# Kernel tuning notes

Measured on AMD Instinct MI355X. Metric: run time of the kernel, lower is better.

Reference implementation:

```python
import jax, jax.numpy as jnp
import numpy as np

DIM = 256
D_STATE = 32
EXPAND = 2
E = EXPAND * DIM            # d_inner = 512
DT_RANK = (DIM + 15) // 16  # 16 (mamba default ceil(d_model/16))
D_CONV = 4                  # mamba default causal conv width
B = 4
L = 1024


def layernorm(x, g, b, eps=1e-5):
    m = jnp.mean(x, axis=-1, keepdims=True)
    v = jnp.var(x, axis=-1, keepdims=True)
    return (x - m) / jnp.sqrt(v + eps) * g + b


def dwconv(x_bcl, w, b, pad):
    # x_bcl: [B,C,L], w: [C,1,K] depthwise
    y = jax.lax.conv_general_dilated(
        x_bcl, w, window_strides=(1,), padding=[pad],
        feature_group_count=x_bcl.shape[1],
        dimension_numbers=('NCW', 'OIW', 'NCW'))
    return y + b[None, :, None]


def selective_scan(u, dt, A, Bm, Cm, D):
    # u,dt: [B,L,E]; A: [E,N]; Bm,Cm: [B,L,N]; D: [E]
    dA = jnp.exp(dt[..., None] * A)                                # [B,L,E,N]
    dBu = dt[..., None] * Bm[:, :, None, :] * u[..., None]         # [B,L,E,N]

    def step(h, inp):
        dA_t, dBu_t = inp
        h = dA_t * h + dBu_t
        return h, h

    h0 = jnp.zeros((u.shape[0], E, D_STATE), u.dtype)
    _, hs = jax.lax.scan(step, h0, (dA.transpose(1, 0, 2, 3), dBu.transpose(1, 0, 2, 3)))
    y = jnp.einsum('lben,bln->ble', hs, Cm)                        # [B,L,E]
    return y + u * D


def mamba(x, in_proj_w, ssm_conv_w, ssm_conv_b, x_proj_w,
          dt_proj_w, dt_proj_b, A_log, Dp, out_proj_w):
    xz = x @ in_proj_w.T                     # [B,L,2E]
    xin, z = xz[..., :E], xz[..., E:]
    # causal depthwise conv (pad left D_CONV-1) + SiLU
    xc = dwconv(xin.transpose(0, 2, 1), ssm_conv_w, ssm_conv_b, (D_CONV - 1, 0))
    u = jax.nn.silu(xc).transpose(0, 2, 1)   # [B,L,E]
    dbl = u @ x_proj_w.T                      # [B,L,dt_rank+2N]
    dt_r = dbl[..., :DT_RANK]
    Bm = dbl[..., DT_RANK:DT_RANK + D_STATE]
    Cm = dbl[..., DT_RANK + D_STATE:]
    dt = jax.nn.softplus(dt_r @ dt_proj_w.T + dt_proj_b)  # [B,L,E]
    A = -jnp.exp(A_log)                                    # [E,N]
    y = selective_scan(u, dt, A, Bm, Cm, Dp)
    y = y * jax.nn.silu(z)
    return y @ out_proj_w.T


def setup_inputs() -> dict:
    key = jax.random.key(0)
    ks = jax.random.split(key, 12)
    f = lambda k, s, sc=0.02: jax.random.normal(k, s, jnp.float32) * sc
    dt_init = jnp.exp(jax.random.uniform(ks[10], (E,), jnp.float32,
                                         np.log(1e-3), np.log(1e-1)))
    dt_bias = dt_init + jnp.log(-jnp.expm1(-dt_init))  # inverse softplus
    A_log = jnp.log(jnp.tile(jnp.arange(1, D_STATE + 1, dtype=jnp.float32), (E, 1)))
    return {
        'x': jax.random.normal(ks[0], (B, L, DIM), jnp.float32),
        'norm1_g': jnp.ones((DIM,), jnp.float32), 'norm1_b': jnp.zeros((DIM,), jnp.float32),
        'conv_w': f(ks[1], (DIM, 1, 3), 0.1), 'conv_b': jnp.zeros((DIM,), jnp.float32),
        'in_proj_w': f(ks[2], (2 * E, DIM)),
        'ssm_conv_w': f(ks[3], (E, 1, D_CONV), 0.1), 'ssm_conv_b': jnp.zeros((E,), jnp.float32),
        'x_proj_w': f(ks[4], (DT_RANK + 2 * D_STATE, E)),
        'dt_proj_w': f(ks[5], (E, DT_RANK), 0.1), 'dt_proj_b': dt_bias,
        'A_log': A_log, 'Dp': jnp.ones((E,), jnp.float32),
        'out_proj_w': f(ks[6], (DIM, E)),
        'norm2_g': jnp.ones((DIM,), jnp.float32), 'norm2_b': jnp.zeros((DIM,), jnp.float32),
        'mlp_w1': f(ks[7], (4 * DIM, DIM)), 'mlp_b1': jnp.zeros((4 * DIM,), jnp.float32),
        'mlp_w2': f(ks[8], (DIM, 4 * DIM)), 'mlp_b2': jnp.zeros((DIM,), jnp.float32),
    }


def reference(x, norm1_g, norm1_b, conv_w, conv_b, in_proj_w, ssm_conv_w,
              ssm_conv_b, x_proj_w, dt_proj_w, dt_proj_b, A_log, Dp,
              out_proj_w, norm2_g, norm2_b, mlp_w1, mlp_b1, mlp_w2, mlp_b2):
    res = x
    h = layernorm(x, norm1_g, norm1_b)
    # local depthwise conv, kernel 3, same padding
    h_conv = dwconv(h.transpose(0, 2, 1), conv_w, conv_b, (1, 1)).transpose(0, 2, 1)
    h = mamba(h_conv + h, in_proj_w, ssm_conv_w, ssm_conv_b, x_proj_w,
              dt_proj_w, dt_proj_b, A_log, Dp, out_proj_w)
    h = res + h  # drop_path = identity (eval)
    m = layernorm(h, norm2_g, norm2_b)
    m = jax.nn.gelu(m @ mlp_w1.T + mlp_b1, approximate=False) @ mlp_w2.T + mlp_b2
    return h + m
```

## Files before the change

### kernel.cpp

```cpp
#include <hip/hip_runtime.h>
#include <hip/hip_bf16.h>
#include <math.h>

#define BATCH 4
#define LSEQ  1024
#define DIM   256
#define ESZ   512
#define NST   32
#define RNK   16
#define MROWS 4096
#define NCH   64
#define CHL   16

typedef __attribute__((ext_vector_type(8))) short bf16x8;
typedef __attribute__((ext_vector_type(4))) float f32x4;

__device__ __forceinline__ float silu_f(float v) { return v / (1.f + __expf(-v)); }
__device__ __forceinline__ float softplus_f(float v) {
    return (v > 20.f) ? v : log1pf(__expf(v));
}

__global__ __launch_bounds__(256) void prep_kernel(
    const float* __restrict__ ipw, const float* __restrict__ opw,
    const float* __restrict__ w1,  const float* __restrict__ w2,
    const float* __restrict__ xpw, __hip_bfloat16* __restrict__ dst,
    const float* __restrict__ x, const float* __restrict__ g,
    const float* __restrict__ b, const float* __restrict__ cw,
    const float* __restrict__ cb, __hip_bfloat16* __restrict__ hm)
{
    if (blockIdx.x < 936) {
        int i = blockIdx.x * 256 + threadIdx.x;
        if (i >= 239616) return;
        const float* s; int off;
        if      (i < 65536)  { s = ipw; off = i; }
        else if (i < 98304)  { s = opw; off = i - 65536; }
        else if (i < 163840) { s = w1;  off = i - 98304; }
        else if (i < 229376) { s = w2;  off = i - 163840; }
        else                 { s = xpw; off = i - 229376; }
        float4 v = ((const float4*)s)[off];
        union { __hip_bfloat16 h[4]; short4 s4; } u;
        u.h[0] = __float2bfloat16(v.x);
        u.h[1] = __float2bfloat16(v.y);
        u.h[2] = __float2bfloat16(v.z);
        u.h[3] = __float2bfloat16(v.w);
        ((short4*)dst)[i] = u.s4;
        return;
    }
    const int row = blockIdx.x - 936;
    const int l   = row & (LSEQ - 1);
    const int d   = threadIdx.x;
    const float gc = g[d], bc = b[d];

    float xc = x[row * DIM + d];
    float xl = (l > 0)        ? x[(row - 1) * DIM + d] : 0.f;
    float xr = (l < LSEQ - 1) ? x[(row + 1) * DIM + d] : 0.f;

    float a[6] = { xc, xc * xc, xl, xl * xl, xr, xr * xr };
    #pragma unroll
    for (int o = 32; o > 0; o >>= 1)
        #pragma unroll
        for (int j = 0; j < 6; ++j) a[j] += __shfl_down(a[j], o, 64);
    __shared__ float red[4][6];
    if ((d & 63) == 0)
        #pragma unroll
        for (int j = 0; j < 6; ++j) red[d >> 6][j] = a[j];
    __syncthreads();
    float t[6];
    #pragma unroll
    for (int j = 0; j < 6; ++j)
        t[j] = red[0][j] + red[1][j] + red[2][j] + red[3][j];

    auto ln = [&](float v, float s, float s2) {
        float m  = s * (1.f / DIM);
        float vr = s2 * (1.f / DIM) - m * m;
        return (v - m) * rsqrtf(vr + 1e-5f) * gc + bc;
    };
    float ln_c = ln(xc, t[0], t[1]);
    float acc  = cw[d * 3 + 1] * ln_c + cb[d] + ln_c;
    if (l > 0)        acc += cw[d * 3 + 0] * ln(xl, t[2], t[3]);
    if (l < LSEQ - 1) acc += cw[d * 3 + 2] * ln(xr, t[4], t[5]);
    hm[row * DIM + d] = __float2bfloat16(acc);
}

__global__ __launch_bounds__(256) void ln_kernel(
    const float* __restrict__ x, const float* __restrict__ g,
    const float* __restrict__ b, __hip_bfloat16* __restrict__ y)
{
    const int row = blockIdx.x;
    const int tid = threadIdx.x;
    float v = x[row * DIM + tid];
    float s = v, s2 = v * v;
    #pragma unroll
    for (int o = 32; o > 0; o >>= 1) {
        s  += __shfl_down(s,  o, 64);
        s2 += __shfl_down(s2, o, 64);
    }
    __shared__ float ls[4], ls2[4];
    if ((tid & 63) == 0) { ls[tid >> 6] = s; ls2[tid >> 6] = s2; }
    __syncthreads();
    float ts  = ls[0]  + ls[1]  + ls[2]  + ls[3];
    float ts2 = ls2[0] + ls2[1] + ls2[2] + ls2[3];
    float mean = ts * (1.f / DIM);
    float var  = ts2 * (1.f / DIM) - mean * mean;
    float inv  = rsqrtf(var + 1e-5f);
    y[row * DIM + tid] =
        __float2bfloat16((v - mean) * inv * g[tid] + b[tid]);
}

__global__ __launch_bounds__(256) void conv4_silu_kernel(
    const __hip_bfloat16* __restrict__ xz, const float* __restrict__ w,
    const float* __restrict__ cb, __hip_bfloat16* __restrict__ ub)
{
    const int i  = blockIdx.x * 256 + threadIdx.x;
    const int e  = i & (ESZ - 1);
    const int bl = i >> 9;
    const int l  = bl & (LSEQ - 1);
    float acc = cb[e];
    #pragma unroll
    for (int k = 0; k < 4; ++k) {
        int ls = l + k - 3;
        if (ls >= 0)
            acc += w[e * 4 + k] * __bfloat162float(xz[(long)(bl + k - 3) * 1024 + e]);
    }
    ub[(long)bl * ESZ + e] = __float2bfloat16(silu_f(acc));
}

__global__ __launch_bounds__(256) void dt_kernel(
    const float* __restrict__ dbl, const float* __restrict__ dtw,
    const float* __restrict__ dtb, __hip_bfloat16* __restrict__ dtf)
{
    const int row = blockIdx.x;
    __shared__ float dr[RNK];
    if (threadIdx.x < RNK) dr[threadIdx.x] = dbl[(long)row * 80 + threadIdx.x];
    __syncthreads();
    #pragma unroll
    for (int hh = 0; hh < 2; ++hh) {
        const int e = threadIdx.x + hh * 256;
        float raw = dtb[e];
        #pragma unroll
        for (int qd = 0; qd < 4; ++qd) {
            float4 w4 = *(const float4*)(dtw + e * RNK + qd * 4);
            raw += w4.x * dr[qd * 4 + 0] + w4.y * dr[qd * 4 + 1]
                 + w4.z * dr[qd * 4 + 2] + w4.w * dr[qd * 4 + 3];
        }
        dtf[(long)row * ESZ + e] = __float2bfloat16(softplus_f(raw));
    }
}

#define EPI_NONE      0
#define EPI_GELU      2
#define EPI_RES       3
#define EPI_BIAS_RES  4

template <int BM, int BN, int EPI, int OUT_BF16>
__global__ __launch_bounds__(256) void gemm_lds(
    const __hip_bfloat16* __restrict__ A, int lda,
    const __hip_bfloat16* __restrict__ W, int ldw,
    void* __restrict__ Cout, int ldc, int K,
    const float* __restrict__ bias,
    const float* __restrict__ res, int ldres)
{
    constexpr int BK  = 64;
    constexpr int WTN = BN / 4;
    constexpr int BNF = WTN / 16;
    constexpr int AMF = BM / 16;
    constexpr int AIT = (BM * 8) / 256;
    constexpr int WIT = (BN * 8) / 256;

    __shared__ __hip_bfloat16 As[2][BM * BK];
    __shared__ __hip_bfloat16 Ws[2][BN * BK];

    const int tid  = threadIdx.x;
    const int lane = tid & 63;
    const int wave = tid >> 6;
    const int wn   = wave * WTN;
    const int m0   = blockIdx.x * BM;
    const int n0   = blockIdx.y * BN;
    const int q    = lane >> 4;
    const int lr   = lane & 15;

    const __hip_bfloat16* Ab = A + (long)m0 * lda;
    const __hip_bfloat16* Wb = W + (long)n0 * ldw;

    f32x4 acc[AMF][BNF];
    #pragma unroll
    for (int i = 0; i < AMF; ++i)
        #pragma unroll
        for (int j = 0; j < BNF; ++j)
            acc[i][j] = (f32x4){0.f, 0.f, 0.f, 0.f};

    auto stage = [&](int s, int k0) {
        #pragma unroll
        for (int it = 0; it < AIT; ++it) {
            const int g = it * 256 + tid;
            __builtin_amdgcn_global_load_lds(
                (const __attribute__((address_space(1))) void*)
                    (Ab + (long)(g >> 3) * lda + k0 + (g & 7) * 8),
                (__attribute__((address_space(3))) void*)
                    (&As[s][(it * 256 + wave * 64) * 8]),
                16, 0, 0);
        }
        #pragma unroll
        for (int it = 0; it < WIT; ++it) {
            const int g = it * 256 + tid;
            __builtin_amdgcn_global_load_lds(
                (const __attribute__((address_space(1))) void*)
                    (Wb + (long)(g >> 3) * ldw + k0 + (g & 7) * 8),
                (__attribute__((address_space(3))) void*)
                    (&Ws[s][(it * 256 + wave * 64) * 8]),
                16, 0, 0);
        }
    };

    stage(0, 0);
    __syncthreads();

    int cur = 0;
    for (int k0 = 0; k0 < K; k0 += BK) {
        if (k0 + BK < K) stage(cur ^ 1, k0 + BK);
        #pragma unroll
        for (int ks = 0; ks < 2; ++ks) {
            bf16x8 af[AMF], bfr[BNF];
            #pragma unroll
            for (int i = 0; i < AMF; ++i)
                af[i] = *(const bf16x8*)(&As[cur][(i * 16 + lr) * BK + ks * 32 + q * 8]);
            #pragma unroll
            for (int j = 0; j < BNF; ++j)
                bfr[j] = *(const bf16x8*)(&Ws[cur][(wn + j * 16 + lr) * BK + ks * 32 + q * 8]);
            #pragma unroll
            for (int i = 0; i < AMF; ++i)
                #pragma unroll
                for (int j = 0; j < BNF; ++j)
                    acc[i][j] = __builtin_amdgcn_mfma_f32_16x16x32_bf16(
                        af[i], bfr[j], acc[i][j], 0, 0, 0);
        }
        __syncthreads();
        cur ^= 1;
    }

    #pragma unroll
    for (int i = 0; i < AMF; ++i) {
        #pragma unroll
        for (int j = 0; j < BNF; ++j) {
            const int col  = n0 + wn + j * 16 + lr;
            const int rowb = m0 + i * 16 + q * 4;
            #pragma unroll
            for (int r = 0; r < 4; ++r) {
                const int row = rowb + r;
                float v = acc[i][j][r];
                if (EPI == EPI_GELU) {
                    v += bias[col];
                    v = 0.5f * v * (1.f + erff(v * 0.70710678118654752f));
                } else if (EPI == EPI_RES) {
                    v += res[(long)row * ldres + col];
                } else if (EPI == EPI_BIAS_RES) {
                    v += bias[col] + res[(long)row * ldres + col];
                }
                if (OUT_BF16)
                    ((__hip_bfloat16*)Cout)[(long)row * ldc + col] = __float2bfloat16(v);
                else
                    ((float*)Cout)[(long)row * ldc + col] = v;
            }
        }
    }
}

__global__ __launch_bounds__(256) void xproj_mfma(
    const __hip_bfloat16* __restrict__ A,
    const __hip_bfloat16* __restrict__ W,
    float* __restrict__ C)
{
    constexpr int LS = 72;
    __shared__ __hip_bfloat16 As[64 * LS];
    __shared__ __hip_bfloat16 Ws[80 * LS];
    const int tid  = threadIdx.x;
    const int lane = tid & 63;
    const int wave = tid >> 6;
    const int wm   = wave * 16;
    const int m0   = blockIdx.x * 64;
    const int srow = tid >> 3;
    const int scol = (tid & 7) * 8;
    const int q    = lane >> 4;
    const int lr   = lane & 15;

    f32x4 acc[5];
    #pragma unroll
    for (int j = 0; j < 5; ++j) acc[j] = (f32x4){0.f, 0.f, 0.f, 0.f};

    float4 ar[2], wr[3];
    #pragma unroll
    for (int r = 0; r < 2; ++r)
        ar[r] = *(const float4*)(A + (long)(m0 + r * 32 + srow) * 512 + scol);
    #pragma unroll
    for (int r = 0; r < 3; ++r) {
        int row = r * 32 + srow;
        wr[r] = (row < 80) ? *(const float4*)(W + (long)row * 512 + scol)
                           : make_float4(0.f, 0.f, 0.f, 0.f);
    }

    for (int k0 = 0; k0 < 512; k0 += 64) {
        __syncthreads();
        #pragma unroll
        for (int r = 0; r < 2; ++r)
            *(float4*)(&As[(r * 32 + srow) * LS + scol]) = ar[r];
        #pragma unroll
        for (int r = 0; r < 3; ++r) {
            int row = r * 32 + srow;
            if (row < 80) *(float4*)(&Ws[row * LS + scol]) = wr[r];
        }
        __syncthreads();
        if (k0 + 64 < 512) {
            #pragma unroll
            for (int r = 0; r < 2; ++r)
                ar[r] = *(const float4*)(A + (long)(m0 + r * 32 + srow) * 512 + k0 + 64 + scol);
            #pragma unroll
            for (int r = 0; r < 3; ++r) {
                int row = r * 32 + srow;
                if (row < 80)
                    wr[r] = *(const float4*)(W + (long)row * 512 + k0 + 64 + scol);
            }
        }
        #pragma unroll
        for (int ks = 0; ks < 2; ++ks) {
            bf16x8 af = *(const bf16x8*)(&As[(wm + lr) * LS + ks * 32 + q * 8]);
            #pragma unroll
            for (int j = 0; j < 5; ++j) {
                bf16x8 bf = *(const bf16x8*)(&Ws[(j * 16 + lr) * LS + ks * 32 + q * 8]);
                acc[j] = __builtin_amdgcn_mfma_f32_16x16x32_bf16(af, bf, acc[j], 0, 0, 0);
            }
        }
    }
    #pragma unroll
    for (int j = 0; j < 5; ++j)
        #pragma unroll
        for (int r = 0; r < 4; ++r)
            C[(long)(m0 + wm + q * 4 + r) * 80 + j * 16 + lr] = acc[j][r];
}

__global__ __launch_bounds__(256) void scan_s1(
    const __hip_bfloat16* __restrict__ xz, const float* __restrict__ dbl,
    const __hip_bfloat16* __restrict__ dtf, const float* __restrict__ A_log,
    const float* __restrict__ scw, const float* __restrict__ scb,
    __hip_bfloat16* __restrict__ P, __hip_bfloat16* __restrict__ Q)
{
    const int tid = threadIdx.x;
    const int e  = ((blockIdx.x & 1) << 8) + tid;
    const int bc = blockIdx.x >> 1;
    const int c  = bc & (NCH - 1);
    const int b  = bc >> 6;

    __shared__ float sBC[CHL][64];
    {
        const int r  = tid >> 4;
        const int cg = (tid & 15) * 4;
        *(float4*)&sBC[r][cg] =
            *(const float4*)(dbl + ((long)b * LSEQ + c * CHL + r) * 80 + 16 + cg);
    }

    float Aen[NST];
    #pragma unroll
    for (int qd = 0; qd < 8; ++qd) {
        float4 a4 = *(const float4*)(A_log + e * NST + qd * 4);
        Aen[qd * 4 + 0] = -__expf(a4.x);
        Aen[qd * 4 + 1] = -__expf(a4.y);
        Aen[qd * 4 + 2] = -__expf(a4.z);
        Aen[qd * 4 + 3] = -__expf(a4.w);
    }
    float cw4[4];
    #pragma unroll
    for (int k = 0; k < 4; ++k) cw4[k] = scw[e * 4 + k];
    const float cbe = scb[e];

    const int l0 = c * CHL;
    const long rowbase = ((long)b * LSEQ) * 1024 + e;
    float xw0, xw1, xw2;
    if (c == 0) { xw0 = xw1 = xw2 = 0.f; }
    else {
        xw0 = __bfloat162float(xz[rowbase + (long)(l0 - 3) * 1024]);
        xw1 = __bfloat162float(xz[rowbase + (long)(l0 - 2) * 1024]);
        xw2 = __bfloat162float(xz[rowbase + (long)(l0 - 1) * 1024]);
    }

    float Pv[NST], Qv[NST];
    #pragma unroll
    for (int n = 0; n < NST; ++n) { Pv[n] = 1.f; Qv[n] = 0.f; }
    __syncthreads();

    for (int t = 0; t < CHL; ++t) {
        const int l = l0 + t;
        const long bl = (long)b * LSEQ + l;
        float xw3 = __bfloat162float(xz[rowbase + (long)l * 1024]);
        float u = silu_f(cbe + cw4[0]*xw0 + cw4[1]*xw1 + cw4[2]*xw2 + cw4[3]*xw3);
        xw0 = xw1; xw1 = xw2; xw2 = xw3;

        float dt = __bfloat162float(dtf[bl * ESZ + e]);
        float xx = dt * u;

        #pragma unroll
        for (int qd = 0; qd < 8; ++qd) {
            float4 b4 = *(const float4*)&sBC[t][qd * 4];
            #pragma unroll
            for (int j = 0; j < 4; ++j) {
                const int n = qd * 4 + j;
                float bn = (j == 0) ? b4.x : (j == 1) ? b4.y : (j == 2) ? b4.z : b4.w;
                float dA = __expf(dt * Aen[n]);
                Pv[n] *= dA;
                Qv[n] = fmaf(dA, Qv[n], xx * bn);
            }
        }
    }
    const long pb = ((long)(b * NCH + c) * NST) * ESZ + e;
    #pragma unroll
    for (int n = 0; n < NST; ++n) {
        P[pb + (long)n * ESZ] = __float2bfloat16(Pv[n]);
        Q[pb + (long)n * ESZ] = __float2bfloat16(Qv[n]);
    }
}

__global__ __launch_bounds__(256) void scan_s2(
    __hip_bfloat16* __restrict__ P, const __hip_bfloat16* __restrict__ Q)
{
    const int tg = blockIdx.x * 256 + threadIdx.x;
    const int e  = tg & (ESZ - 1);
    const int n  = (tg >> 9) & (NST - 1);
    const int b  = tg >> 14;
    float h = 0.f;
    #pragma unroll 4
    for (int c = 0; c < NCH; ++c) {
        const long idx = ((long)(b * NCH + c) * NST + n) * ESZ + e;
        float Pv = __bfloat162float(P[idx]);
        float Qv = __bfloat162float(Q[idx]);
        P[idx] = __float2bfloat16(h);
        h = fmaf(Pv, h, Qv);
    }
}

__global__ __launch_bounds__(256) void scan_s3(
    const __hip_bfloat16* __restrict__ xz, const float* __restrict__ dbl,
    const __hip_bfloat16* __restrict__ dtf, const float* __restrict__ A_log,
    const float* __restrict__ scw, const float* __restrict__ scb,
    const float* __restrict__ Dp, const __hip_bfloat16* __restrict__ H,
    __hip_bfloat16* __restrict__ yg)
{
    const int tid = threadIdx.x;
    const int e  = ((blockIdx.x & 1) << 8) + tid;
    const int bc = blockIdx.x >> 1;
    const int c  = bc & (NCH - 1);
    const int b  = bc >> 6;

    __shared__ float sBC[CHL][64];
    {
        const int r  = tid >> 4;
        const int cg = (tid & 15) * 4;
        *(float4*)&sBC[r][cg] =
            *(const float4*)(dbl + ((long)b * LSEQ + c * CHL + r) * 80 + 16 + cg);
    }

    float Aen[NST];
    #pragma unroll
    for (int qd = 0; qd < 8; ++qd) {
        float4 a4 = *(const float4*)(A_log + e * NST + qd * 4);
        Aen[qd * 4 + 0] = -__expf(a4.x);
        Aen[qd * 4 + 1] = -__expf(a4.y);
        Aen[qd * 4 + 2] = -__expf(a4.z);
        Aen[qd * 4 + 3] = -__expf(a4.w);
    }
    float cw4[4];
    #pragma unroll
    for (int k = 0; k < 4; ++k) cw4[k] = scw[e * 4 + k];
    const float cbe = scb[e];
    const float dpe = Dp[e];

    float h[NST];
    const long pb = ((long)(b * NCH + c) * NST) * ESZ + e;
    #pragma unroll
    for (int n = 0; n < NST; ++n)
        h[n] = __bfloat162float(H[pb + (long)n * ESZ]);

    const int l0 = c * CHL;
    const long rowbase = ((long)b * LSEQ) * 1024 + e;
    float xw0, xw1, xw2;
    if (c == 0) { xw0 = xw1 = xw2 = 0.f; }
    else {
        xw0 = __bfloat162float(xz[rowbase + (long)(l0 - 3) * 1024]);
        xw1 = __bfloat162float(xz[rowbase + (long)(l0 - 2) * 1024]);
        xw2 = __bfloat162float(xz[rowbase + (long)(l0 - 1) * 1024]);
    }
    __syncthreads();

    for (int t = 0; t < CHL; ++t) {
        const int l = l0 + t;
        const long bl = (long)b * LSEQ + l;
        float xw3 = __bfloat162float(xz[rowbase + (long)l * 1024]);
        float u = silu_f(cbe + cw4[0]*xw0 + cw4[1]*xw1 + cw4[2]*xw2 + cw4[3]*xw3);
        xw0 = xw1; xw1 = xw2; xw2 = xw3;

        float dt = __bfloat162float(dtf[bl * ESZ + e]);
        float xx = dt * u;

        float y = 0.f;
        #pragma unroll
        for (int qd = 0; qd < 8; ++qd) {
            float4 b4 = *(const float4*)&sBC[t][qd * 4];
            float4 c4 = *(const float4*)&sBC[t][32 + qd * 4];
            #pragma unroll
            for (int j = 0; j < 4; ++j) {
                const int n = qd * 4 + j;
                float bn = (j == 0) ? b4.x : (j == 1) ? b4.y : (j == 2) ? b4.z : b4.w;
                float cn = (j == 0) ? c4.x : (j == 1) ? c4.y : (j == 2) ? c4.z : c4.w;
                float dA = __expf(dt * Aen[n]);
                h[n] = fmaf(dA, h[n], xx * bn);
                y = fmaf(h[n], cn, y);
            }
        }
        y += u * dpe;
        float z = __bfloat162float(xz[rowbase + (long)l * 1024 + ESZ]);
        yg[bl * ESZ + e] = __float2bfloat16(y * silu_f(z));
    }
}

extern "C" void kernel_launch(void* const* d_in, const int* in_sizes, int n_in,
                              void* d_out, int out_size, void* d_ws, size_t ws_size,
                              hipStream_t stream)
{
    const float* x    = (const float*)d_in[0];
    const float* n1g  = (const float*)d_in[1];
    const float* n1b  = (const float*)d_in[2];
    const float* cw   = (const float*)d_in[3];
    const float* cb   = (const float*)d_in[4];
    const float* ipw  = (const float*)d_in[5];
    const float* scw  = (const float*)d_in[6];
    const float* scb  = (const float*)d_in[7];
    const float* xpw  = (const float*)d_in[8];
    const float* dtw  = (const float*)d_in[9];
    const float* dtbi = (const float*)d_in[10];
    const float* alog = (const float*)d_in[11];
    const float* dp   = (const float*)d_in[12];
    const float* opw  = (const float*)d_in[13];
    const float* n2g  = (const float*)d_in[14];
    const float* n2b  = (const float*)d_in[15];
    const float* w1   = (const float*)d_in[16];
    const float* b1   = (const float*)d_in[17];
    const float* w2   = (const float*)d_in[18];
    const float* b2   = (const float*)d_in[19];
    float* out = (float*)d_out;

    float* ws = (float*)d_ws;
    __hip_bfloat16* hmb  = (__hip_bfloat16*)(ws + 0);
    __hip_bfloat16* xzb  = (__hip_bfloat16*)(ws + 524288);
    __hip_bfloat16* ub   = (__hip_bfloat16*)(ws + 2621440);
    float*          dbl  = ws + 3670016;
    __hip_bfloat16* dtf  = (__hip_bfloat16*)(ws + 3997696);
    __hip_bfloat16* P    = (__hip_bfloat16*)(ws + 5046272);
    __hip_bfloat16* Q    = (__hip_bfloat16*)(ws + 7143424);
    __hip_bfloat16* ygb  = (__hip_bfloat16*)(ws + 9240576);
    float*          hres = ws + 10289152;
    __hip_bfloat16* h1b  = (__hip_bfloat16*)(ws + 11337728);
    __hip_bfloat16* midb = (__hip_bfloat16*)(ws + 11862016);
    __hip_bfloat16* wb   = (__hip_bfloat16*)(ws + 13959168);
    __hip_bfloat16* ipwb = wb;
    __hip_bfloat16* opwb = wb + 262144;
    __hip_bfloat16* w1b  = wb + 393216;
    __hip_bfloat16* w2b  = wb + 655360;
    __hip_bfloat16* xpwb = wb + 917504;

    prep_kernel<<<5032, 256, 0, stream>>>(ipw, opw, w1, w2, xpw, wb,
                                          x, n1g, n1b, cw, cb, hmb);
    gemm_lds<64, 128, EPI_NONE, 1><<<dim3(64, 8), 256, 0, stream>>>(
        hmb, 256, ipwb, 256, xzb, 1024, 256, nullptr, nullptr, 0);
    conv4_silu_kernel<<<8192, 256, 0, stream>>>(xzb, scw, scb, ub);
    xproj_mfma<<<64, 256, 0, stream>>>(ub, xpwb, dbl);
    dt_kernel<<<MROWS, 256, 0, stream>>>(dbl, dtw, dtbi, dtf);
    scan_s1<<<512, 256, 0, stream>>>(xzb, dbl, dtf, alog, scw, scb, P, Q);
    scan_s2<<<256, 256, 0, stream>>>(P, Q);
    scan_s3<<<512, 256, 0, stream>>>(xzb, dbl, dtf, alog, scw, scb, dp, P, ygb);
    gemm_lds<64, 64, EPI_RES, 0><<<dim3(64, 4), 256, 0, stream>>>(
        ygb, 512, opwb, 512, hres, 256, 512, nullptr, x, 256);
    ln_kernel<<<MROWS, 256, 0, stream>>>(hres, n2g, n2b, h1b);
    gemm_lds<64, 128, EPI_GELU, 1><<<dim3(64, 8), 256, 0, stream>>>(
        h1b, 256, w1b, 256, midb, 1024, 256, b1, nullptr, 0);
    gemm_lds<64, 64, EPI_BIAS_RES, 0><<<dim3(64, 4), 256, 0, stream>>>(
        midb, 1024, w2b, 1024, out, 256, 1024, b2, hres, 256);
}
```

Measured before the change: 237.7 us.

## Fuse dt projection and softplus into scan kernels; shrink GEMM tiles

Removes the standalone dt_kernel and its bf16 dt buffer. The scan_s1 and scan_s3 kernels now load all 80 dbl columns per chunk into LDS and compute the rank-16 dt projection plus softplus inline. This drops one launch and a 4096x512 write/read round trip, but recomputes dt in both scan passes. Separately, GEMM tile sizes are reduced (64x128 to 64x64, 64x64 to 32x64) to launch more blocks on the device.

```diff
diff --git a/kernel.cpp b/kernel.cpp
--- a/kernel.cpp
+++ b/kernel.cpp
@@ -125,28 +125,6 @@
     ub[(long)bl * ESZ + e] = __float2bfloat16(silu_f(acc));
 }
 
-__global__ __launch_bounds__(256) void dt_kernel(
-    const float* __restrict__ dbl, const float* __restrict__ dtw,
-    const float* __restrict__ dtb, __hip_bfloat16* __restrict__ dtf)
-{
-    const int row = blockIdx.x;
-    __shared__ float dr[RNK];
-    if (threadIdx.x < RNK) dr[threadIdx.x] = dbl[(long)row * 80 + threadIdx.x];
-    __syncthreads();
-    #pragma unroll
-    for (int hh = 0; hh < 2; ++hh) {
-        const int e = threadIdx.x + hh * 256;
-        float raw = dtb[e];
-        #pragma unroll
-        for (int qd = 0; qd < 4; ++qd) {
-            float4 w4 = *(const float4*)(dtw + e * RNK + qd * 4);
-            raw += w4.x * dr[qd * 4 + 0] + w4.y * dr[qd * 4 + 1]
-                 + w4.z * dr[qd * 4 + 2] + w4.w * dr[qd * 4 + 3];
-        }
-        dtf[(long)row * ESZ + e] = __float2bfloat16(softplus_f(raw));
-    }
-}
-
 #define EPI_NONE      0
 #define EPI_GELU      2
 #define EPI_RES       3
@@ -339,7 +317,8 @@
 
 __global__ __launch_bounds__(256) void scan_s1(
     const __hip_bfloat16* __restrict__ xz, const float* __restrict__ dbl,
-    const __hip_bfloat16* __restrict__ dtf, const float* __restrict__ A_log,
+    const float* __restrict__ dtw, const float* __restrict__ dtb,
+    const float* __restrict__ A_log,
     const float* __restrict__ scw, const float* __restrict__ scb,
     __hip_bfloat16* __restrict__ P, __hip_bfloat16* __restrict__ Q)
 {
@@ -349,12 +328,11 @@
     const int c  = bc & (NCH - 1);
     const int b  = bc >> 6;
 
-    __shared__ float sBC[CHL][64];
-    {
-        const int r  = tid >> 4;
-        const int cg = (tid & 15) * 4;
-        *(float4*)&sBC[r][cg] =
-            *(const float4*)(dbl + ((long)b * LSEQ + c * CHL + r) * 80 + 16 + cg);
+    __shared__ float sD[CHL][80];
+    for (int g = tid; g < CHL * 20; g += 256) {
+        int r = g / 20, cg = (g % 20) * 4;
+        *(float4*)&sD[r][cg] =
+            *(const float4*)(dbl + ((long)b * LSEQ + c * CHL + r) * 80 + cg);
     }
 
     float Aen[NST];
@@ -370,6 +348,12 @@
     #pragma unroll
     for (int k = 0; k < 4; ++k) cw4[k] = scw[e * 4 + k];
     const float cbe = scb[e];
+
+    float4 wq[4];
+    #pragma unroll
+    for (int qd = 0; qd < 4; ++qd)
+        wq[qd] = *(const float4*)(dtw + e * RNK + qd * 4);
+    const float dtbe = dtb[e];
 
     const int l0 = c * CHL;
     const long rowbase = ((long)b * LSEQ) * 1024 + e;
@@ -388,17 +372,25 @@
 
     for (int t = 0; t < CHL; ++t) {
         const int l = l0 + t;
-        const long bl = (long)b * LSEQ + l;
         float xw3 = __bfloat162float(xz[rowbase + (long)l * 1024]);
         float u = silu_f(cbe + cw4[0]*xw0 + cw4[1]*xw1 + cw4[2]*xw2 + cw4[3]*xw3);
         xw0 = xw1; xw1 = xw2; xw2 = xw3;
 
-        float dt = __bfloat162float(dtf[bl * ESZ + e]);
+        float4 d0 = *(const float4*)&sD[t][0];
+        float4 d1 = *(const float4*)&sD[t][4];
+        float4 d2 = *(const float4*)&sD[t][8];
+        float4 d3 = *(const float4*)&sD[t][12];
+        float raw = dtbe
+            + wq[0].x*d0.x + wq[0].y*d0.y + wq[0].z*d0.z + wq[0].w*d0.w
+            + wq[1].x*d1.x + wq[1].y*d1.y + wq[1].z*d1.z + wq[1].w*d1.w
+            + wq[2].x*d2.x + wq[2].y*d2.y + wq[2].z*d2.z + wq[2].w*d2.w
+            + wq[3].x*d3.x + wq[3].y*d3.y + wq[3].z*d3.z + wq[3].w*d3.w;
+        float dt = softplus_f(raw);
         float xx = dt * u;
 
         #pragma unroll
         for (int qd = 0; qd < 8; ++qd) {
-            float4 b4 = *(const float4*)&sBC[t][qd * 4];
+            float4 b4 = *(const float4*)&sD[t][16 + qd * 4];
             #pragma unroll
             for (int j = 0; j < 4; ++j) {
                 const int n = qd * 4 + j;
@@ -437,7 +429,8 @@
 
 __global__ __launch_bounds__(256) void scan_s3(
     const __hip_bfloat16* __restrict__ xz, const float* __restrict__ dbl,
-    const __hip_bfloat16* __restrict__ dtf, const float* __restrict__ A_log,
+    const float* __restrict__ dtw, const float* __restrict__ dtb,
+    const float* __restrict__ A_log,
     const float* __restrict__ scw, const float* __restrict__ scb,
     const float* __restrict__ Dp, const __hip_bfloat16* __restrict__ H,
     __hip_bfloat16* __restrict__ yg)
@@ -448,12 +441,11 @@
     const int c  = bc & (NCH - 1);
     const int b  = bc >> 6;
 
-    __shared__ float sBC[CHL][64];
-    {
-        const int r  = tid >> 4;
-        const int cg = (tid & 15) * 4;
-        *(float4*)&sBC[r][cg] =
-            *(const float4*)(dbl + ((long)b * LSEQ + c * CHL + r) * 80 + 16 + cg);
+    __shared__ float sD[CHL][80];
+    for (int g = tid; g < CHL * 20; g += 256) {
+        int r = g / 20, cg = (g % 20) * 4;
+        *(float4*)&sD[r][cg] =
+            *(const float4*)(dbl + ((long)b * LSEQ + c * CHL + r) * 80 + cg);
     }
 
     float Aen[NST];
@@ -470,6 +462,12 @@
     for (int k = 0; k < 4; ++k) cw4[k] = scw[e * 4 + k];
     const float cbe = scb[e];
     const float dpe = Dp[e];
+
+    float4 wq[4];
+    #pragma unroll
+    for (int qd = 0; qd < 4; ++qd)
+        wq[qd] = *(const float4*)(dtw + e * RNK + qd * 4);
+    const float dtbe = dtb[e];
 
     float h[NST];
     const long pb = ((long)(b * NCH + c) * NST) * ESZ + e;
@@ -495,14 +493,23 @@
         float u = silu_f(cbe + cw4[0]*xw0 + cw4[1]*xw1 + cw4[2]*xw2 + cw4[3]*xw3);
         xw0 = xw1; xw1 = xw2; xw2 = xw3;
 
-        float dt = __bfloat162float(dtf[bl * ESZ + e]);
+        float4 d0 = *(const float4*)&sD[t][0];
+        float4 d1 = *(const float4*)&sD[t][4];
+        float4 d2 = *(const float4*)&sD[t][8];
+        float4 d3 = *(const float4*)&sD[t][12];
+        float raw = dtbe
+            + wq[0].x*d0.x + wq[0].y*d0.y + wq[0].z*d0.z + wq[0].w*d0.w
+            + wq[1].x*d1.x + wq[1].y*d1.y + wq[1].z*d1.z + wq[1].w*d1.w
+            + wq[2].x*d2.x + wq[2].y*d2.y + wq[2].z*d2.z + wq[2].w*d2.w
+            + wq[3].x*d3.x + wq[3].y*d3.y + wq[3].z*d3.z + wq[3].w*d3.w;
+        float dt = softplus_f(raw);
         float xx = dt * u;
 
         float y = 0.f;
         #pragma unroll
         for (int qd = 0; qd < 8; ++qd) {
-            float4 b4 = *(const float4*)&sBC[t][qd * 4];
-            float4 c4 = *(const float4*)&sBC[t][32 + qd * 4];
+            float4 b4 = *(const float4*)&sD[t][16 + qd * 4];
+            float4 c4 = *(const float4*)&sD[t][48 + qd * 4];
             #pragma unroll
             for (int j = 0; j < 4; ++j) {
                 const int n = qd * 4 + j;
@@ -550,7 +557,6 @@
     __hip_bfloat16* xzb  = (__hip_bfloat16*)(ws + 524288);
     __hip_bfloat16* ub   = (__hip_bfloat16*)(ws + 2621440);
     float*          dbl  = ws + 3670016;
-    __hip_bfloat16* dtf  = (__hip_bfloat16*)(ws + 3997696);
     __hip_bfloat16* P    = (__hip_bfloat16*)(ws + 5046272);
     __hip_bfloat16* Q    = (__hip_bfloat16*)(ws + 7143424);
     __hip_bfloat16* ygb  = (__hip_bfloat16*)(ws + 9240576);
@@ -566,19 +572,18 @@
 
     prep_kernel<<<5032, 256, 0, stream>>>(ipw, opw, w1, w2, xpw, wb,
                                           x, n1g, n1b, cw, cb, hmb);
-    gemm_lds<64, 128, EPI_NONE, 1><<<dim3(64, 8), 256, 0, stream>>>(
+    gemm_lds<64, 64, EPI_NONE, 1><<<dim3(64, 16), 256, 0, stream>>>(
         hmb, 256, ipwb, 256, xzb, 1024, 256, nullptr, nullptr, 0);
     conv4_silu_kernel<<<8192, 256, 0, stream>>>(xzb, scw, scb, ub);
     xproj_mfma<<<64, 256, 0, stream>>>(ub, xpwb, dbl);
-    dt_kernel<<<MROWS, 256, 0, stream>>>(dbl, dtw, dtbi, dtf);
-    scan_s1<<<512, 256, 0, stream>>>(xzb, dbl, dtf, alog, scw, scb, P, Q);
+    scan_s1<<<512, 256, 0, stream>>>(xzb, dbl, dtw, dtbi, alog, scw, scb, P, Q);
     scan_s2<<<256, 256, 0, stream>>>(P, Q);
-    scan_s3<<<512, 256, 0, stream>>>(xzb, dbl, dtf, alog, scw, scb, dp, P, ygb);
-    gemm_lds<64, 64, EPI_RES, 0><<<dim3(64, 4), 256, 0, stream>>>(
+    scan_s3<<<512, 256, 0, stream>>>(xzb, dbl, dtw, dtbi, alog, scw, scb, dp, P, ygb);
+    gemm_lds<32, 64, EPI_RES, 0><<<dim3(128, 4), 256, 0, stream>>>(
         ygb, 512, opwb, 512, hres, 256, 512, nullptr, x, 256);
     ln_kernel<<<MROWS, 256, 0, stream>>>(hres, n2g, n2b, h1b);
-    gemm_lds<64, 128, EPI_GELU, 1><<<dim3(64, 8), 256, 0, stream>>>(
+    gemm_lds<64, 64, EPI_GELU, 1><<<dim3(64, 16), 256, 0, stream>>>(
         h1b, 256, w1b, 256, midb, 1024, 256, b1, nullptr, 0);
-    gemm_lds<64, 64, EPI_BIAS_RES, 0><<<dim3(64, 4), 256, 0, stream>>>(
+    gemm_lds<32, 64, EPI_BIAS_RES, 0><<<dim3(128, 4), 256, 0, stream>>>(
         midb, 1024, w2b, 1024, out, 256, 1024, b2, hres, 256);
 }
```

Result: slower. 244.8 us (+3.0%).
